# Kernel tuning notes

Hardware: AMD Instinct MI355X
Metric: run time of the kernel (lower is better)

Reference implementation:

```python
import jax, jax.numpy as jnp
import numpy as np

HIDDEN = 2048
NUM_HEADS = 16
NUM_KV_HEADS = 4
HEAD_DIM = HIDDEN // NUM_HEADS            # 128
Q_PER_KV = NUM_HEADS // NUM_KV_HEADS      # 4
GROUP_SIZE = (Q_PER_KV + 2) * HEAD_DIM    # 768
TOTAL_PROJ = NUM_KV_HEADS * GROUP_SIZE    # 3072
SEQ, BATCH = 2048, 2


def setup_inputs() -> dict:
    key = jax.random.key(0)
    k1, k2, k3 = jax.random.split(key, 3)
    x = jax.random.normal(k1, (SEQ, BATCH, HIDDEN), dtype=jnp.float32)
    weight_qkv = jax.random.normal(k2, (TOTAL_PROJ, HIDDEN), dtype=jnp.float32) * 0.02
    weight_proj = jax.random.normal(k3, (HIDDEN, NUM_HEADS * HEAD_DIM), dtype=jnp.float32) * 0.02
    return {"x": x, "weight_qkv": weight_qkv, "weight_proj": weight_proj}


def reference(x, weight_qkv, weight_proj):
    seq, batch, hidden = x.shape
    q_size = Q_PER_KV * HEAD_DIM

    # fused grouped QKV projection: [S*B, TOTAL_PROJ]
    qkv = x.reshape(-1, hidden) @ weight_qkv.T
    qkv = qkv.reshape(-1, NUM_KV_HEADS, GROUP_SIZE)
    q = qkv[:, :, :q_size].reshape(seq, batch, NUM_HEADS, HEAD_DIM)
    k = qkv[:, :, q_size:q_size + HEAD_DIM].reshape(seq, batch, NUM_KV_HEADS, HEAD_DIM)
    v = qkv[:, :, q_size + HEAD_DIM:].reshape(seq, batch, NUM_KV_HEADS, HEAD_DIM)

    # GQA: repeat_interleave kv heads to match q heads
    k = jnp.repeat(k, Q_PER_KV, axis=2)
    v = jnp.repeat(v, Q_PER_KV, axis=2)

    # [b, h, s, d]
    q = q.transpose(1, 2, 0, 3)
    k = k.transpose(1, 2, 0, 3)
    v = v.transpose(1, 2, 0, 3)

    scale = 1.0 / np.sqrt(HEAD_DIM)
    scores = jnp.einsum('bhqd,bhkd->bhqk', q, k) * scale
    causal = jnp.tril(jnp.ones((seq, seq), dtype=bool))
    scores = jnp.where(causal, scores, jnp.float32(-jnp.inf))
    probs = jax.nn.softmax(scores, axis=-1)
    attn = jnp.einsum('bhqk,bhkd->bhqd', probs, v)

    # back to [s, b, h*d] then output projection
    attn = attn.transpose(2, 0, 1, 3).reshape(seq * batch, NUM_HEADS * HEAD_DIM)
    out = attn @ weight_proj.T
    return out.reshape(seq, batch, hidden)
```

## Files before the change

### kernel.cpp

```cpp
#include <hip/hip_runtime.h>

#define SEQ 2048
#define BATCH 2
#define HIDDEN 2048
#define NHEADS 16
#define NKV 4
#define HD 128
#define GROUP 768
#define TPROJ 3072
#define NTOK (SEQ*BATCH)

typedef __attribute__((ext_vector_type(8))) __bf16 bf16x8;
typedef __attribute__((ext_vector_type(8))) unsigned short ushort8_t;
typedef __attribute__((ext_vector_type(4))) float f32x4;

union U8cast { ushort8_t u; bf16x8 b; };
__device__ inline bf16x8 as_bf(ushort8_t u) { U8cast c; c.u = u; return c.b; }

union Bf16U { __bf16 h; unsigned short u; };

__device__ inline unsigned short f2bf(float f) {
    unsigned int u = __float_as_uint(f);
    return (unsigned short)((u + 0x7FFFu + ((u >> 16) & 1u)) >> 16);
}

__device__ inline ushort8_t load8_f32_bf16(const float* __restrict__ p) {
    float4 v0 = *(const float4*)p;
    float4 v1 = *(const float4*)(p + 4);
    ushort8_t u;
    u[0] = f2bf(v0.x); u[1] = f2bf(v0.y); u[2] = f2bf(v0.z); u[3] = f2bf(v0.w);
    u[4] = f2bf(v1.x); u[5] = f2bf(v1.y); u[6] = f2bf(v1.z); u[7] = f2bf(v1.w);
    return u;
}

__device__ inline float exp2a(float x) {
    float r; asm("v_exp_f32 %0, %1" : "=v"(r) : "v"(x)); return r;
}

__device__ inline void gload_lds16(const unsigned short* g, unsigned short* l) {
    __builtin_amdgcn_global_load_lds(
        (const __attribute__((address_space(1))) void*)g,
        (__attribute__((address_space(3))) void*)l, 16, 0, 0);
}

#define CONV_N0 ((size_t)NTOK * HIDDEN)
#define CONV_N1 ((size_t)TPROJ * HIDDEN)
#define CONV_N2 ((size_t)HIDDEN * HIDDEN)
__global__ __launch_bounds__(256) void conv3_kernel(
    const float* __restrict__ x, const float* __restrict__ wq, const float* __restrict__ wp,
    unsigned short* __restrict__ xb, unsigned short* __restrict__ wqb, unsigned short* __restrict__ wpb)
{
    size_t i = (size_t)(blockIdx.x * 256 + threadIdx.x) * 8;
    if (i < CONV_N0) {
        *(ushort8_t*)(xb + i) = load8_f32_bf16(x + i);
    } else if (i < CONV_N0 + CONV_N1) {
        size_t j = i - CONV_N0;
        *(ushort8_t*)(wqb + j) = load8_f32_bf16(wq + j);
    } else {
        size_t j = i - CONV_N0 - CONV_N1;
        *(ushort8_t*)(wpb + j) = load8_f32_bf16(wp + j);
    }
}

template<bool OUT_BF16>
__global__ __launch_bounds__(512, 2) void gemm256_kernel(
    const unsigned short* __restrict__ A, const unsigned short* __restrict__ B,
    void* __restrict__ Cv, int M, int N, int K)
{
    __shared__ unsigned short lds[2][2][256 * 64];

    const int t = threadIdx.x, lane = t & 63, w = t >> 6;
    const int wm = w >> 2, wn = w & 3;
    const int l16 = lane & 15, lg = lane >> 4;

    const int cpx = (int)gridDim.x >> 3;
    const int wg  = ((int)blockIdx.x & 7) * cpx + ((int)blockIdx.x >> 3);
    const int nbn = N >> 8;
    const int m0 = (wg / nbn) << 8, n0 = (wg % nbn) << 8;
    const int NKT = K >> 6;

    const int srow = lane >> 3;
    const int scol = ((lane & 7) ^ srow) << 3;

    f32x4 acc[8][4] = {};

    auto stage = [&](const unsigned short* __restrict__ G, int g0, int kt, int op) {
        const int k0 = kt << 6;
        unsigned short* Ld = lds[kt & 1][op];
#pragma unroll
        for (int i = 0; i < 4; ++i) {
            const int r = w * 32 + i * 8;
            gload_lds16(G + (size_t)(g0 + r + srow) * K + k0 + scol, Ld + r * 64);
        }
    };

    stage(A, m0, 0, 0); stage(B, n0, 0, 1);
    stage(A, m0, 1, 0); stage(B, n0, 1, 1);

    for (int kt = 0; kt < NKT; ++kt) {
        const unsigned short* As_ = lds[kt & 1][0];
        const unsigned short* Bs_ = lds[kt & 1][1];

        if (kt < NKT - 1) asm volatile("s_waitcnt vmcnt(8)" ::: "memory");
        else              asm volatile("s_waitcnt vmcnt(0)" ::: "memory");
        __builtin_amdgcn_sched_barrier(0);
        __builtin_amdgcn_s_barrier();
        __builtin_amdgcn_sched_barrier(0);

        bf16x8 aR[8], b0R[4], b1R[4];

#pragma unroll
        for (int i = 0; i < 4; ++i)
#pragma unroll
            for (int s = 0; s < 2; ++s) {
                int row  = wm * 128 + i * 16 + l16;
                int slot = ((s << 2) | lg) ^ (l16 & 7);
                aR[i * 2 + s] = as_bf(*(const ushort8_t*)&As_[row * 64 + slot * 8]);
            }
#pragma unroll
        for (int j = 0; j < 2; ++j)
#pragma unroll
            for (int s = 0; s < 2; ++s) {
                int row  = wn * 64 + j * 16 + l16;
                int slot = ((s << 2) | lg) ^ (l16 & 7);
                b0R[j * 2 + s] = as_bf(*(const ushort8_t*)&Bs_[row * 64 + slot * 8]);
            }
        __builtin_amdgcn_s_setprio(1);
#pragma unroll
        for (int i = 0; i < 4; ++i)
#pragma unroll
            for (int j = 0; j < 2; ++j)
#pragma unroll
                for (int s = 0; s < 2; ++s)
                    acc[i][j] = __builtin_amdgcn_mfma_f32_16x16x32_bf16(aR[i*2+s], b0R[j*2+s], acc[i][j], 0, 0, 0);
        __builtin_amdgcn_s_setprio(0);

#pragma unroll
        for (int j = 0; j < 2; ++j)
#pragma unroll
            for (int s = 0; s < 2; ++s) {
                int row  = wn * 64 + 32 + j * 16 + l16;
                int slot = ((s << 2) | lg) ^ (l16 & 7);
                b1R[j * 2 + s] = as_bf(*(const ushort8_t*)&Bs_[row * 64 + slot * 8]);
            }
        __builtin_amdgcn_s_setprio(1);
#pragma unroll
        for (int i = 0; i < 4; ++i)
#pragma unroll
            for (int j = 0; j < 2; ++j)
#pragma unroll
                for (int s = 0; s < 2; ++s)
                    acc[i][2 + j] = __builtin_amdgcn_mfma_f32_16x16x32_bf16(aR[i*2+s], b1R[j*2+s], acc[i][2 + j], 0, 0, 0);
        __builtin_amdgcn_s_setprio(0);

        __builtin_amdgcn_sched_barrier(0);
        __builtin_amdgcn_s_barrier();
        __builtin_amdgcn_sched_barrier(0);
        if (kt + 2 < NKT) stage(B, n0, kt + 2, 1);
        __builtin_amdgcn_sched_barrier(0);

#pragma unroll
        for (int i = 0; i < 4; ++i)
#pragma unroll
            for (int s = 0; s < 2; ++s) {
                int row  = wm * 128 + 64 + i * 16 + l16;
                int slot = ((s << 2) | lg) ^ (l16 & 7);
                aR[i * 2 + s] = as_bf(*(const ushort8_t*)&As_[row * 64 + slot * 8]);
            }
        __builtin_amdgcn_s_setprio(1);
#pragma unroll
        for (int i = 0; i < 4; ++i)
#pragma unroll
            for (int j = 0; j < 2; ++j)
#pragma unroll
                for (int s = 0; s < 2; ++s)
                    acc[4 + i][2 + j] = __builtin_amdgcn_mfma_f32_16x16x32_bf16(aR[i*2+s], b1R[j*2+s], acc[4 + i][2 + j], 0, 0, 0);
        __builtin_amdgcn_s_setprio(0);

        __builtin_amdgcn_sched_barrier(0);
        __builtin_amdgcn_s_barrier();
        __builtin_amdgcn_sched_barrier(0);
        if (kt + 2 < NKT) stage(A, m0, kt + 2, 0);
        __builtin_amdgcn_sched_barrier(0);

        __builtin_amdgcn_s_setprio(1);
#pragma unroll
        for (int i = 0; i < 4; ++i)
#pragma unroll
            for (int j = 0; j < 2; ++j)
#pragma unroll
                for (int s = 0; s < 2; ++s)
                    acc[4 + i][j] = __builtin_amdgcn_mfma_f32_16x16x32_bf16(aR[i*2+s], b0R[j*2+s], acc[4 + i][j], 0, 0, 0);
        __builtin_amdgcn_s_setprio(0);
    }

#pragma unroll
    for (int ia = 0; ia < 8; ++ia)
#pragma unroll
        for (int jb = 0; jb < 4; ++jb)
#pragma unroll
            for (int r = 0; r < 4; ++r) {
                int row = m0 + wm * 128 + (ia >> 2) * 64 + (ia & 3) * 16 + lg * 4 + r;
                int col = n0 + wn * 64 + (jb >> 1) * 32 + (jb & 1) * 16 + l16;
                if (OUT_BF16)
                    ((unsigned short*)Cv)[(size_t)row * N + col] = f2bf(acc[ia][jb][r]);
                else
                    ((float*)Cv)[(size_t)row * N + col] = acc[ia][jb][r];
            }
}

__global__ __launch_bounds__(256) void vtrans_kernel(const unsigned short* __restrict__ qkv,
                                                     unsigned short* __restrict__ vT)
{
    const int t = threadIdx.x;
    const int s0 = blockIdx.x * 128 + (t & 15) * 8;
    const int bk = blockIdx.y;
    const int b_idx = bk >> 2;
    const int voff = (bk & 3) * GROUP + 640;
    const int d0 = (t >> 4) * 8;
    ushort8_t in[8];
#pragma unroll
    for (int j = 0; j < 8; ++j)
        in[j] = *(const ushort8_t*)(qkv + (size_t)((s0 + j) * BATCH + b_idx) * TPROJ + voff + d0);
#pragma unroll
    for (int dd = 0; dd < 8; ++dd) {
        ushort8_t ov;
#pragma unroll
        for (int j = 0; j < 8; ++j) ov[j] = in[j][dd];
        *(ushort8_t*)(vT + (size_t)(bk * HD + d0 + dd) * SEQ + s0) = ov;
    }
}

__global__ __launch_bounds__(256, 2) void attn_kernel(const unsigned short* __restrict__ qkv,
                                                      const unsigned short* __restrict__ vT,
                                                      unsigned short* __restrict__ attn_out)
{
    __shared__ unsigned short Ks[2][64][128];
    __shared__ unsigned short Vt[2][128][64];
    __shared__ __align__(16) unsigned short Plds[4][16][72];

    const int t = threadIdx.x, lane = t & 63, w = t >> 6;
    const int l16 = lane & 15, lg = lane >> 4;

    const int bid = (int)blockIdx.x;
    const int qt  = 127 - (bid >> 3);
    const int bk  = bid & 7;
    const int b_idx = bk >> 2;
    const int kvh   = bk & 3;
    const int qb0   = qt * 16;
    const int qoff  = kvh * GROUP + w * HD;
    const int koff  = kvh * GROUP + 512;
    const int vrow0 = (b_idx * NKV + kvh) * HD;
    const int h     = kvh * 4 + w;

    const float SCL2 = 0.08838834764831845f * 1.44269504f;
    const float THRU = 8.0f / SCL2;

    ushort8_t qf[4];
    {
        size_t qrow = (size_t)((qb0 + l16) * BATCH + b_idx) * TPROJ + qoff;
#pragma unroll
        for (int kc = 0; kc < 4; ++kc)
            qf[kc] = *(const ushort8_t*)(qkv + qrow + kc * 32 + lg * 8);
    }

    f32x4 o[8] = {};
    float mstate[4], lstate[4], negm2[4];
#pragma unroll
    for (int r = 0; r < 4; ++r) { mstate[r] = -1e30f; lstate[r] = 0.f; negm2[r] = 0.f; }

    const int nIter = (qt >> 2) + 1;

    auto stageKV = [&](int it) {
        const int buf = it & 1;
        const int kv0 = it << 6;
#pragma unroll
        for (int i = 0; i < 4; ++i) {
            int rl = w * 16 + i * 4 + (lane >> 4);
            int g  = (lane & 15) ^ (rl & 7);
            gload_lds16(qkv + (size_t)((kv0 + rl) * BATCH + b_idx) * TPROJ + koff + g * 8,
                        &Ks[buf][w * 16 + i * 4][0]);
        }
#pragma unroll
        for (int i = 0; i < 4; ++i) {
            int rl = w * 32 + i * 8 + (lane >> 3);
            int g  = (lane & 7) ^ ((lane >> 3) & 7);
            gload_lds16(vT + (size_t)(vrow0 + rl) * SEQ + kv0 + g * 8,
                        &Vt[buf][w * 32 + i * 8][0]);
        }
    };

    stageKV(0);
    if (nIter > 1) stageKV(1);

    for (int it = 0; it < nIter; ++it) {
        const int buf = it & 1;
        const int kv0 = it * 64;

        if (it + 1 < nIter) asm volatile("s_waitcnt vmcnt(8)" ::: "memory");
        else                asm volatile("s_waitcnt vmcnt(0)" ::: "memory");
        __builtin_amdgcn_sched_barrier(0);
        __builtin_amdgcn_s_barrier();
        __builtin_amdgcn_sched_barrier(0);

        f32x4 s[4] = {};
        __builtin_amdgcn_s_setprio(1);
#pragma unroll
        for (int nf = 0; nf < 4; ++nf)
#pragma unroll
            for (int kc = 0; kc < 4; ++kc) {
                int phys = (kc * 4 + lg) ^ (l16 & 7);
                ushort8_t kb = *(const ushort8_t*)&Ks[buf][nf * 16 + l16][phys * 8];
                s[nf] = __builtin_amdgcn_mfma_f32_16x16x32_bf16(as_bf(qf[kc]), as_bf(kb), s[nf], 0, 0, 0);
            }
        __builtin_amdgcn_s_setprio(0);

        if (it == nIter - 1) {
#pragma unroll
            for (int nf = 0; nf < 4; ++nf)
#pragma unroll
                for (int r = 0; r < 4; ++r) {
                    int kv_g = kv0 + l16 + 16 * nf;
                    int q_g  = qb0 + lg * 4 + r;
                    if (kv_g > q_g) s[nf][r] = -1e30f;
                }
        }

        float rmax[4];
#pragma unroll
        for (int r = 0; r < 4; ++r)
            rmax[r] = fmaxf(fmaxf(s[0][r], s[1][r]), fmaxf(s[2][r], s[3][r]));
#pragma unroll
        for (int msk = 1; msk <= 8; msk <<= 1)
#pragma unroll
            for (int r = 0; r < 4; ++r) rmax[r] = fmaxf(rmax[r], __shfl_xor(rmax[r], msk));

        float g = -1e30f;
#pragma unroll
        for (int r = 0; r < 4; ++r) g = fmaxf(g, rmax[r] - mstate[r]);
        if (!__all(g <= THRU)) {
#pragma unroll
            for (int r = 0; r < 4; ++r) {
                float mn = fmaxf(mstate[r], rmax[r]);
                float corr = exp2a((mstate[r] - mn) * SCL2);
                mstate[r] = mn;
                negm2[r]  = -mn * SCL2;
                lstate[r] *= corr;
#pragma unroll
                for (int f = 0; f < 8; ++f) o[f][r] *= corr;
            }
        }

        float rsum[4] = {};
#pragma unroll
        for (int nf = 0; nf < 4; ++nf)
#pragma unroll
            for (int r = 0; r < 4; ++r) {
                float p = exp2a(fmaf(s[nf][r], SCL2, negm2[r]));
                rsum[r] += p;
                Bf16U cv; cv.h = (__bf16)p;
                Plds[w][lg * 4 + r][l16 + 16 * nf] = cv.u;
            }
#pragma unroll
        for (int msk = 1; msk <= 8; msk <<= 1)
#pragma unroll
            for (int r = 0; r < 4; ++r) rsum[r] += __shfl_xor(rsum[r], msk);
#pragma unroll
        for (int r = 0; r < 4; ++r) lstate[r] += rsum[r];

        __builtin_amdgcn_s_setprio(1);
#pragma unroll
        for (int c = 0; c < 2; ++c) {
            ushort8_t pf = *(const ushort8_t*)&Plds[w][l16][c * 32 + lg * 8];
#pragma unroll
            for (int f = 0; f < 8; ++f) {
                int phys = (c * 4 + lg) ^ (l16 & 7);
                ushort8_t vf = *(const ushort8_t*)&Vt[buf][l16 + 16 * f][phys * 8];
                o[f] = __builtin_amdgcn_mfma_f32_16x16x32_bf16(as_bf(pf), as_bf(vf), o[f], 0, 0, 0);
            }
        }
        __builtin_amdgcn_s_setprio(0);

        __builtin_amdgcn_sched_barrier(0);
        __builtin_amdgcn_s_barrier();
        __builtin_amdgcn_sched_barrier(0);
        if (it + 2 < nIter) stageKV(it + 2);
    }

    float linv[4];
#pragma unroll
    for (int r = 0; r < 4; ++r) linv[r] = 1.0f / lstate[r];
#pragma unroll
    for (int f = 0; f < 8; ++f)
#pragma unroll
        for (int r = 0; r < 4; ++r) {
            int q_g = qb0 + lg * 4 + r;
            size_t row = (size_t)(q_g * BATCH + b_idx) * HIDDEN;
            attn_out[row + h * HD + 16 * f + l16] = f2bf(o[f][r] * linv[r]);
        }
}

extern "C" void kernel_launch(void* const* d_in, const int* in_sizes, int n_in,
                              void* d_out, int out_size, void* d_ws, size_t ws_size,
                              hipStream_t stream) {
    const float* x     = (const float*)d_in[0];
    const float* wqkv  = (const float*)d_in[1];
    const float* wproj = (const float*)d_in[2];
    float* out = (float*)d_out;

    unsigned short* qkv   = (unsigned short*)d_ws;
    unsigned short* attn  = qkv  + (size_t)NTOK * TPROJ;
    unsigned short* vT    = attn + (size_t)NTOK * HIDDEN;
    unsigned short* xb    = vT   + (size_t)BATCH * NKV * HD * SEQ;
    unsigned short* wqkvb = xb   + (size_t)NTOK * HIDDEN;
    unsigned short* wprojb= wqkvb+ (size_t)TPROJ * HIDDEN;

    conv3_kernel<<<dim3((unsigned)((CONV_N0 + CONV_N1 + CONV_N2) / 2048)), 256, 0, stream>>>(
        x, wqkv, wproj, xb, wqkvb, wprojb);

    gemm256_kernel<true><<<dim3((NTOK / 256) * (TPROJ / 256)), 512, 0, stream>>>(
        xb, wqkvb, (void*)qkv, NTOK, TPROJ, HIDDEN);

    vtrans_kernel<<<dim3(SEQ / 128, BATCH * NKV), 256, 0, stream>>>(qkv, vT);

    attn_kernel<<<dim3(1024), 256, 0, stream>>>(qkv, vT, attn);

    gemm256_kernel<false><<<dim3((NTOK / 256) * (HIDDEN / 256)), 512, 0, stream>>>(
        attn, wprojb, (void*)out, NTOK, HIDDEN, HIDDEN);
}
```

Baseline: 216.1 us.

## Compute transposed QK^T and keep P in registers, removing the LDS round-trip

```diff
diff --git a/kernel.cpp b/kernel.cpp
--- a/kernel.cpp
+++ b/kernel.cpp
@@ -237,7 +237,6 @@
 {
     __shared__ unsigned short Ks[2][64][128];
     __shared__ unsigned short Vt[2][128][64];
-    __shared__ __align__(16) unsigned short Plds[4][16][72];
 
     const int t = threadIdx.x, lane = t & 63, w = t >> 6;
     const int l16 = lane & 15, lg = lane >> 4;
@@ -265,9 +264,7 @@
     }
 
     f32x4 o[8] = {};
-    float mstate[4], lstate[4], negm2[4];
-#pragma unroll
-    for (int r = 0; r < 4; ++r) { mstate[r] = -1e30f; lstate[r] = 0.f; negm2[r] = 0.f; }
+    float mstate = -1e30f, lstate = 0.f, negm2 = 0.f;
 
     const int nIter = (qt >> 2) + 1;
 
@@ -277,8 +274,9 @@
 #pragma unroll
         for (int i = 0; i < 4; ++i) {
             int rl = w * 16 + i * 4 + (lane >> 4);
+            int pr = 32 * ((rl >> 4) & 1) + 8 * ((rl >> 2) & 3) + 4 * (rl >> 5) + (rl & 3);
             int g  = (lane & 15) ^ (rl & 7);
-            gload_lds16(qkv + (size_t)((kv0 + rl) * BATCH + b_idx) * TPROJ + koff + g * 8,
+            gload_lds16(qkv + (size_t)((kv0 + pr) * BATCH + b_idx) * TPROJ + koff + g * 8,
                         &Ks[buf][w * 16 + i * 4][0]);
         }
 #pragma unroll
@@ -311,74 +309,77 @@
             for (int kc = 0; kc < 4; ++kc) {
                 int phys = (kc * 4 + lg) ^ (l16 & 7);
                 ushort8_t kb = *(const ushort8_t*)&Ks[buf][nf * 16 + l16][phys * 8];
-                s[nf] = __builtin_amdgcn_mfma_f32_16x16x32_bf16(as_bf(qf[kc]), as_bf(kb), s[nf], 0, 0, 0);
+                s[nf] = __builtin_amdgcn_mfma_f32_16x16x32_bf16(as_bf(kb), as_bf(qf[kc]), s[nf], 0, 0, 0);
             }
         __builtin_amdgcn_s_setprio(0);
 
         if (it == nIter - 1) {
+            const int q_g = qb0 + l16;
 #pragma unroll
             for (int nf = 0; nf < 4; ++nf)
 #pragma unroll
                 for (int r = 0; r < 4; ++r) {
-                    int kv_g = kv0 + l16 + 16 * nf;
-                    int q_g  = qb0 + lg * 4 + r;
+                    int kv_g = kv0 + 32 * (nf & 1) + 8 * lg + 4 * (nf >> 1) + r;
                     if (kv_g > q_g) s[nf][r] = -1e30f;
                 }
         }
 
-        float rmax[4];
-#pragma unroll
-        for (int r = 0; r < 4; ++r)
-            rmax[r] = fmaxf(fmaxf(s[0][r], s[1][r]), fmaxf(s[2][r], s[3][r]));
-#pragma unroll
-        for (int msk = 1; msk <= 8; msk <<= 1)
-#pragma unroll
-            for (int r = 0; r < 4; ++r) rmax[r] = fmaxf(rmax[r], __shfl_xor(rmax[r], msk));
-
-        float g = -1e30f;
-#pragma unroll
-        for (int r = 0; r < 4; ++r) g = fmaxf(g, rmax[r] - mstate[r]);
-        if (!__all(g <= THRU)) {
+        float a0 = fmaxf(fmaxf(s[0][0], s[0][1]), fmaxf(s[0][2], s[0][3]));
+        float a1 = fmaxf(fmaxf(s[1][0], s[1][1]), fmaxf(s[1][2], s[1][3]));
+        float a2 = fmaxf(fmaxf(s[2][0], s[2][1]), fmaxf(s[2][2], s[2][3]));
+        float a3 = fmaxf(fmaxf(s[3][0], s[3][1]), fmaxf(s[3][2], s[3][3]));
+        float rmax = fmaxf(fmaxf(a0, a1), fmaxf(a2, a3));
+        rmax = fmaxf(rmax, __shfl_xor(rmax, 16));
+        rmax = fmaxf(rmax, __shfl_xor(rmax, 32));
+
+        if (!__all(rmax - mstate <= THRU)) {
+            float mn = fmaxf(mstate, rmax);
+            float corr = exp2a((mstate - mn) * SCL2);
+            mstate = mn;
+            negm2  = -mn * SCL2;
+            lstate *= corr;
+            float co[4];
+#pragma unroll
+            for (int r = 0; r < 4; ++r) co[r] = __shfl(corr, 4 * lg + r);
+#pragma unroll
+            for (int f = 0; f < 8; ++f)
+#pragma unroll
+                for (int r = 0; r < 4; ++r) o[f][r] *= co[r];
+        }
+
+        float p[4][4];
+        float rs0 = 0.f, rs1 = 0.f;
+#pragma unroll
+        for (int nf = 0; nf < 4; ++nf)
 #pragma unroll
             for (int r = 0; r < 4; ++r) {
-                float mn = fmaxf(mstate[r], rmax[r]);
-                float corr = exp2a((mstate[r] - mn) * SCL2);
-                mstate[r] = mn;
-                negm2[r]  = -mn * SCL2;
-                lstate[r] *= corr;
-#pragma unroll
-                for (int f = 0; f < 8; ++f) o[f][r] *= corr;
-            }
-        }
-
-        float rsum[4] = {};
-#pragma unroll
-        for (int nf = 0; nf < 4; ++nf)
-#pragma unroll
-            for (int r = 0; r < 4; ++r) {
-                float p = exp2a(fmaf(s[nf][r], SCL2, negm2[r]));
-                rsum[r] += p;
-                Bf16U cv; cv.h = (__bf16)p;
-                Plds[w][lg * 4 + r][l16 + 16 * nf] = cv.u;
-            }
-#pragma unroll
-        for (int msk = 1; msk <= 8; msk <<= 1)
-#pragma unroll
-            for (int r = 0; r < 4; ++r) rsum[r] += __shfl_xor(rsum[r], msk);
-#pragma unroll
-        for (int r = 0; r < 4; ++r) lstate[r] += rsum[r];
-
-        __builtin_amdgcn_s_setprio(1);
-#pragma unroll
-        for (int c = 0; c < 2; ++c) {
-            ushort8_t pf = *(const ushort8_t*)&Plds[w][l16][c * 32 + lg * 8];
+                float pv = exp2a(fmaf(s[nf][r], SCL2, negm2));
+                p[nf][r] = pv;
+                if (nf < 2) rs0 += pv; else rs1 += pv;
+            }
+        float rsum = rs0 + rs1;
+        rsum += __shfl_xor(rsum, 16);
+        rsum += __shfl_xor(rsum, 32);
+        lstate += rsum;
+
+        ushort8_t paf[2];
+#pragma unroll
+        for (int c = 0; c < 2; ++c)
+#pragma unroll
+            for (int e = 0; e < 8; ++e) {
+                Bf16U cv; cv.h = (__bf16)((e < 4) ? p[c][e] : p[2 + c][e - 4]);
+                paf[c][e] = cv.u;
+            }
+
+        __builtin_amdgcn_s_setprio(1);
+#pragma unroll
+        for (int c = 0; c < 2; ++c)
 #pragma unroll
             for (int f = 0; f < 8; ++f) {
                 int phys = (c * 4 + lg) ^ (l16 & 7);
                 ushort8_t vf = *(const ushort8_t*)&Vt[buf][l16 + 16 * f][phys * 8];
-                o[f] = __builtin_amdgcn_mfma_f32_16x16x32_bf16(as_bf(pf), as_bf(vf), o[f], 0, 0, 0);
-            }
-        }
+                o[f] = __builtin_amdgcn_mfma_f32_16x16x32_bf16(as_bf(paf[c]), as_bf(vf), o[f], 0, 0, 0);
+            }
         __builtin_amdgcn_s_setprio(0);
 
         __builtin_amdgcn_sched_barrier(0);
@@ -387,9 +388,10 @@
         if (it + 2 < nIter) stageKV(it + 2);
     }
 
+    float li = 1.0f / lstate;
     float linv[4];
 #pragma unroll
-    for (int r = 0; r < 4; ++r) linv[r] = 1.0f / lstate[r];
+    for (int r = 0; r < 4; ++r) linv[r] = __shfl(li, 4 * lg + r);
 #pragma unroll
     for (int f = 0; f < 8; ++f)
 #pragma unroll
```

Result: faster. 192.8 us (-10.8%).
